# Kernel optimization log

Hardware: AMD Instinct MI355X
Metric: run time of the kernel (lower is better)

## Reference

```python
import jax, jax.numpy as jnp
import numpy as np

N, IN, H, M, C, E = 200000, 256, 256, 64, 64, 3200000

def gelu(x):
    # torch F.gelu default is exact (erf) gelu
    return jax.nn.gelu(x, approximate=False)

def setup_inputs() -> dict:
    key = jax.random.key(0)
    ks = jax.random.split(key, 12)
    s = 0.02  # small init scale for weights
    p = lambda k, shape: jax.random.normal(k, shape, jnp.float32) * s
    inp = {
        "x": jax.random.normal(ks[0], (N, IN), jnp.float32),
        "edge_index": jax.random.randint(ks[1], (2, E), 0, N),
        "ff1_w0": p(ks[2], (IN, H)),   "ff1_b0": jnp.zeros((H,), jnp.float32),
        "wA0":    p(ks[3], (H, H)),    "wB0":    p(ks[4], (H, M)),
        "ff2_w0": p(ks[5], (2 * H, H)),"ff2_b0": jnp.zeros((H,), jnp.float32),
        "ff1_w1": p(ks[6], (H, H)),    "ff1_b1": jnp.zeros((H,), jnp.float32),
        "wA1":    p(ks[7], (H, H)),    "wB1":    p(ks[8], (H, M)),
        "ff2_w1": p(ks[9], (2 * H, H)),"ff2_b1": jnp.zeros((H,), jnp.float32),
        "head_w": p(ks[10], (H, C)),   "head_b": jnp.zeros((C,), jnp.float32),
    }
    return inp

def _ghm_block(X, ff1_w, ff1_b, wA, wB, ff2_w, ff2_b):
    # FF1
    Hf = gelu(X @ ff1_w + ff1_b)                 # (N, h)
    # HyperAggregation: hypernetwork produces token-mixing weights
    W_tar = gelu(Hf @ wA) @ wB                   # (N, m)
    agg = gelu(Hf.T @ W_tar)                     # (h, m) - mixes over nodes
    agg = (agg @ W_tar.T).T                      # (N, h)
    # root connection: concat aggregated with pre-agg features
    agg = gelu(jnp.concatenate([agg, Hf], axis=1))  # (N, 2h)
    return agg @ ff2_w + ff2_b                   # (N, h)

def reference(x, edge_index, ff1_w0, ff1_b0, wA0, wB0, ff2_w0, ff2_b0,
              ff1_w1, ff1_b1, wA1, wB1, ff2_w1, ff2_b1, head_w, head_b):
    # task='graph', batch=None: whole node set is one fully-connected neighborhood
    X = _ghm_block(x, ff1_w0, ff1_b0, wA0, wB0, ff2_w0, ff2_b0)
    X = _ghm_block(X, ff1_w1, ff1_b1, wA1, wB1, ff2_w1, ff2_b1)
    g = jnp.mean(X, axis=0, keepdims=True)       # (1, h)
    return g @ head_w + head_b                   # (1, C)
```

## Files before the change

kernel.cpp:

```cpp
#include <hip/hip_runtime.h>


typedef unsigned short u16;
typedef unsigned int u32;
typedef short bf16x8 __attribute__((ext_vector_type(8)));
typedef float f32x4 __attribute__((ext_vector_type(4)));

__device__ __forceinline__ float gelu_f(float x) {
  float s = x * x;
  float z = x * fmaf(s, -0.10294348f, -2.3022077f);
  float e = __builtin_amdgcn_exp2f(z);
  return x * __builtin_amdgcn_rcpf(1.0f + e);
}
__device__ __forceinline__ u16 f2b(float f) {
  union { float f; unsigned u; } v; v.f = f;
  unsigned u = v.u;
  u += 0x7fffu + ((u >> 16) & 1u);
  return (u16)(u >> 16);
}
__device__ __forceinline__ float b2f(u16 b) {
  union { float f; u32 u; } v; v.u = (u32)b << 16;
  return v.f;
}
__device__ __forceinline__ int swz(int row, int col) {
  return row * 256 + (((col >> 3) ^ (row & 7)) << 3) + (col & 7);
}

__global__ __launch_bounds__(256) void prep_weights(
    const float* __restrict__ s0, const float* __restrict__ s1,
    const float* __restrict__ s2, const float* __restrict__ s3,
    const float* __restrict__ s4, const float* __restrict__ s5,
    const float* __restrict__ s6, const float* __restrict__ s7,
    u16* __restrict__ dst)
{
  int idx = blockIdx.x * 256 + threadIdx.x;
  if (idx >= 557056) return;
  const float* src; int base, R, C;
  if (idx < 278528) {
    if (idx < 131072) {
      if (idx < 65536) { base = 0;      src = s0; R = 256; C = 256; }
      else             { base = 65536;  src = s1; R = 256; C = 256; }
    } else {
      if (idx < 147456){ base = 131072; src = s2; R = 256; C = 64;  }
      else             { base = 147456; src = s3; R = 512; C = 256; }
    }
  } else {
    int j = idx - 278528;
    if (j < 131072) {
      if (j < 65536)   { base = 278528; src = s4; R = 256; C = 256; }
      else             { base = 344064; src = s5; R = 256; C = 256; }
    } else {
      if (j < 147456)  { base = 409600; src = s6; R = 256; C = 64;  }
      else             { base = 425984; src = s7; R = 512; C = 256; }
    }
  }
  int local = idx - base;
  int o = local / R;
  int k = local - o * R;
  dst[idx] = f2b(src[k * C + o]);
}

template<bool AFP32>
__global__ __launch_bounds__(256, 2) void ff1_hyper(
    const void* __restrict__ Av, const u16* __restrict__ W1T,
    const float* __restrict__ bias, const u16* __restrict__ wAT,
    const u16* __restrict__ wBT, u16* __restrict__ Hf,
    u16* __restrict__ Hfg, u16* __restrict__ Wt, int N)
{
  __shared__ u16 Asm[128][264];
  const int tid = threadIdx.x;
  const int wave = tid >> 6, lane = tid & 63;
  int r0 = blockIdx.x * 128;
  if (r0 > N - 128) r0 = N - 128;

  if constexpr (AFP32) {
    const float* A = (const float*)Av;
    #pragma unroll
    for (int j = 0; j < 32; ++j) {
      int idx = j * 256 + tid;
      int row = idx >> 6, c4 = idx & 63;
      float4 v = *(const float4*)(A + (size_t)(r0 + row) * 256 + c4 * 4);
      uint2 p;
      p.x = (u32)f2b(v.x) | ((u32)f2b(v.y) << 16);
      p.y = (u32)f2b(v.z) | ((u32)f2b(v.w) << 16);
      *(uint2*)&Asm[row][c4 * 4] = p;
    }
  } else {
    const u16* A = (const u16*)Av;
    #pragma unroll
    for (int j = 0; j < 16; ++j) {
      int idx = j * 256 + tid;
      int row = idx >> 5, c8 = idx & 31;
      *(uint4*)&Asm[row][c8 * 8] =
          *(const uint4*)(A + (size_t)(r0 + row) * 256 + c8 * 8);
    }
  }
  __syncthreads();

  const int lm = lane & 15, lq = lane >> 4;
  const int n0 = wave * 64;

  f32x4 acc[8][4] = {};
  {
    bf16x8 bb[2][4];
    #pragma unroll
    for (int ct = 0; ct < 4; ++ct)
      bb[0][ct] = *(const bf16x8*)(W1T + (size_t)(n0 + ct * 16 + lm) * 256 + lq * 8);
    #pragma unroll
    for (int s = 0; s < 8; ++s) {
      const int cur = s & 1;
      if (s < 7)
        #pragma unroll
        for (int ct = 0; ct < 4; ++ct)
          bb[cur ^ 1][ct] = *(const bf16x8*)(W1T + (size_t)(n0 + ct * 16 + lm) * 256 + (s + 1) * 32 + lq * 8);
      bf16x8 a[8];
      #pragma unroll
      for (int rt = 0; rt < 8; ++rt)
        a[rt] = *(const bf16x8*)&Asm[rt * 16 + lm][s * 32 + lq * 8];
      #pragma unroll
      for (int rt = 0; rt < 8; ++rt)
        #pragma unroll
        for (int ct = 0; ct < 4; ++ct)
          acc[rt][ct] = __builtin_amdgcn_mfma_f32_16x16x32_bf16(a[rt], bb[cur][ct], acc[rt][ct], 0, 0, 0);
    }
  }
  __syncthreads();

  {
    float bv[4];
    #pragma unroll
    for (int ct = 0; ct < 4; ++ct) bv[ct] = bias[n0 + ct * 16 + lm];
    #pragma unroll
    for (int rt = 0; rt < 8; ++rt)
      #pragma unroll
      for (int ct = 0; ct < 4; ++ct)
        #pragma unroll
        for (int rg = 0; rg < 4; ++rg) {
          float g = gelu_f(acc[rt][ct][rg] + bv[ct]);
          Asm[rt * 16 + lq * 4 + rg][n0 + ct * 16 + lm] = f2b(g);
        }
  }
  __syncthreads();

  #pragma unroll
  for (int j = 0; j < 16; ++j) {
    int idx = j * 256 + tid;
    int row = idx >> 5, c8 = idx & 31;
    uint4 v = *(const uint4*)&Asm[row][c8 * 8];
    *(uint4*)(Hf + (size_t)(r0 + row) * 256 + c8 * 8) = v;
    u32 wsv[4] = {v.x, v.y, v.z, v.w};
    uint4 go;
    u32* gp = (u32*)&go;
    #pragma unroll
    for (int t = 0; t < 4; ++t) {
      float lo = gelu_f(b2f((u16)(wsv[t] & 0xFFFFu)));
      float hi = gelu_f(b2f((u16)(wsv[t] >> 16)));
      gp[t] = (u32)f2b(lo) | ((u32)f2b(hi) << 16);
    }
    *(uint4*)(Hfg + (size_t)(r0 + row) * 256 + c8 * 8) = go;
  }

  #pragma unroll
  for (int rt = 0; rt < 8; ++rt)
    #pragma unroll
    for (int ct = 0; ct < 4; ++ct)
      acc[rt][ct] = (f32x4){0.f, 0.f, 0.f, 0.f};
  {
    bf16x8 bb[2][4];
    #pragma unroll
    for (int ct = 0; ct < 4; ++ct)
      bb[0][ct] = *(const bf16x8*)(wAT + (size_t)(n0 + ct * 16 + lm) * 256 + lq * 8);
    #pragma unroll
    for (int s = 0; s < 8; ++s) {
      const int cur = s & 1;
      if (s < 7)
        #pragma unroll
        for (int ct = 0; ct < 4; ++ct)
          bb[cur ^ 1][ct] = *(const bf16x8*)(wAT + (size_t)(n0 + ct * 16 + lm) * 256 + (s + 1) * 32 + lq * 8);
      bf16x8 a[8];
      #pragma unroll
      for (int rt = 0; rt < 8; ++rt)
        a[rt] = *(const bf16x8*)&Asm[rt * 16 + lm][s * 32 + lq * 8];
      #pragma unroll
      for (int rt = 0; rt < 8; ++rt)
        #pragma unroll
        for (int ct = 0; ct < 4; ++ct)
          acc[rt][ct] = __builtin_amdgcn_mfma_f32_16x16x32_bf16(a[rt], bb[cur][ct], acc[rt][ct], 0, 0, 0);
    }
  }
  __syncthreads();
  #pragma unroll
  for (int rt = 0; rt < 8; ++rt)
    #pragma unroll
    for (int ct = 0; ct < 4; ++ct)
      #pragma unroll
      for (int rg = 0; rg < 4; ++rg)
        Asm[rt * 16 + lq * 4 + rg][n0 + ct * 16 + lm] = f2b(gelu_f(acc[rt][ct][rg]));
  __syncthreads();

  f32x4 acc2[2][4] = {};
  {
    bf16x8 bb[2][4];
    #pragma unroll
    for (int ct = 0; ct < 4; ++ct)
      bb[0][ct] = *(const bf16x8*)(wBT + (size_t)(ct * 16 + lm) * 256 + lq * 8);
    #pragma unroll
    for (int s = 0; s < 8; ++s) {
      const int cur = s & 1;
      if (s < 7)
        #pragma unroll
        for (int ct = 0; ct < 4; ++ct)
          bb[cur ^ 1][ct] = *(const bf16x8*)(wBT + (size_t)(ct * 16 + lm) * 256 + (s + 1) * 32 + lq * 8);
      bf16x8 a[2];
      #pragma unroll
      for (int rt = 0; rt < 2; ++rt)
        a[rt] = *(const bf16x8*)&Asm[wave * 32 + rt * 16 + lm][s * 32 + lq * 8];
      #pragma unroll
      for (int rt = 0; rt < 2; ++rt)
        #pragma unroll
        for (int ct = 0; ct < 4; ++ct)
          acc2[rt][ct] = __builtin_amdgcn_mfma_f32_16x16x32_bf16(a[rt], bb[cur][ct], acc2[rt][ct], 0, 0, 0);
    }
  }
  #pragma unroll
  for (int rt = 0; rt < 2; ++rt)
    #pragma unroll
    for (int ct = 0; ct < 4; ++ct)
      #pragma unroll
      for (int rg = 0; rg < 4; ++rg)
        Asm[wave * 32 + rt * 16 + lq * 4 + rg][ct * 16 + lm] = f2b(acc2[rt][ct][rg]);
  #pragma unroll
  for (int t = 0; t < 4; ++t) {
    int u = t * 64 + lane;
    int rl = u >> 3, c8 = u & 7;
    *(uint4*)(Wt + (size_t)(r0 + wave * 32 + rl) * 64 + c8 * 8) =
        *(const uint4*)&Asm[wave * 32 + rl][c8 * 8];
  }
}

__global__ __launch_bounds__(256, 3) void s_partial_v2(
    const u16* __restrict__ Hf, const u16* __restrict__ Wt,
    float* __restrict__ Spart, int N)
{
  __shared__ u16 HfT[256][72];
  __shared__ u16 WtT[64][72];
  const int tid = threadIdx.x;
  const int wave = tid >> 6, lane = tid & 63;
  const int lm = lane & 15, lq = lane >> 4;
  const int rp = tid & 31;
  const int mb = tid >> 5;
  uint4 hx[4][2], wx[2];
  auto issue = [&](int ch) {
    int i0 = ch << 6;
    #pragma unroll
    for (int q = 0; q < 4; ++q) {
      const u16* px = Hf + (size_t)(i0 + 2 * rp) * 256 + (mb + 8 * q) * 8;
      hx[q][0] = *(const uint4*)px;
      hx[q][1] = *(const uint4*)(px + 256);
    }
    const u16* pw = Wt + (size_t)(i0 + 2 * rp) * 64 + mb * 8;
    wx[0] = *(const uint4*)pw;
    wx[1] = *(const uint4*)(pw + 64);
  };
  f32x4 acc[4][4] = {};
  const int nchunk = N >> 6;
  int ch = blockIdx.x;
  if (ch < nchunk) issue(ch);
  for (; ch < nchunk; ch += gridDim.x) {
    __syncthreads();
    #pragma unroll
    for (int q = 0; q < 4; ++q) {
      int m = mb + 8 * q;
      u32 xs[4] = {hx[q][0].x, hx[q][0].y, hx[q][0].z, hx[q][0].w};
      u32 ys[4] = {hx[q][1].x, hx[q][1].y, hx[q][1].z, hx[q][1].w};
      #pragma unroll
      for (int t = 0; t < 4; ++t) {
        *(u32*)&HfT[m * 8 + 2 * t][2 * rp]     = (xs[t] & 0xFFFFu) | (ys[t] << 16);
        *(u32*)&HfT[m * 8 + 2 * t + 1][2 * rp] = (xs[t] >> 16) | (ys[t] & 0xFFFF0000u);
      }
    }
    {
      u32 xs[4] = {wx[0].x, wx[0].y, wx[0].z, wx[0].w};
      u32 ys[4] = {wx[1].x, wx[1].y, wx[1].z, wx[1].w};
      #pragma unroll
      for (int t = 0; t < 4; ++t) {
        *(u32*)&WtT[mb * 8 + 2 * t][2 * rp]     = (xs[t] & 0xFFFFu) | (ys[t] << 16);
        *(u32*)&WtT[mb * 8 + 2 * t + 1][2 * rp] = (xs[t] >> 16) | (ys[t] & 0xFFFF0000u);
      }
    }
    if (ch + (int)gridDim.x < nchunk) issue(ch + (int)gridDim.x);
    __syncthreads();
    #pragma unroll
    for (int k0 = 0; k0 < 64; k0 += 32) {
      bf16x8 a[4], b[4];
      #pragma unroll
      for (int t = 0; t < 4; ++t)
        a[t] = *(const bf16x8*)&HfT[wave * 64 + t * 16 + lm][k0 + lq * 8];
      #pragma unroll
      for (int m = 0; m < 4; ++m)
        b[m] = *(const bf16x8*)&WtT[m * 16 + lm][k0 + lq * 8];
      #pragma unroll
      for (int t = 0; t < 4; ++t)
        #pragma unroll
        for (int m = 0; m < 4; ++m)
          acc[t][m] = __builtin_amdgcn_mfma_f32_16x16x32_bf16(a[t], b[m], acc[t][m], 0, 0, 0);
    }
  }
  float* out = Spart + (size_t)blockIdx.x * 16384;
  #pragma unroll
  for (int t = 0; t < 4; ++t)
    #pragma unroll
    for (int m = 0; m < 4; ++m)
      #pragma unroll
      for (int rg = 0; rg < 4; ++rg)
        out[(size_t)(wave * 64 + t * 16 + lq * 4 + rg) * 64 + m * 16 + lm] = acc[t][m][rg];
}

__global__ __launch_bounds__(256) void s_reduce(
    const float* __restrict__ Spart, u16* __restrict__ agg, int nparts)
{
  int e = blockIdx.x * 256 + threadIdx.x;
  float s0 = 0.f, s1 = 0.f, s2 = 0.f, s3 = 0.f;
  for (int p = 0; p < nparts; p += 4) {
    s0 += Spart[(size_t)(p + 0) * 16384 + e];
    s1 += Spart[(size_t)(p + 1) * 16384 + e];
    s2 += Spart[(size_t)(p + 2) * 16384 + e];
    s3 += Spart[(size_t)(p + 3) * 16384 + e];
  }
  agg[e] = f2b(gelu_f((s0 + s1) + (s2 + s3)));
}

template<bool COLSUM>
__global__ __launch_bounds__(256, 2) void fused_p_ff2_v6(
    const u16* __restrict__ Wt, const u16* __restrict__ agg,
    const u16* __restrict__ Hfg, const u16* __restrict__ W2T,
    const float* __restrict__ bias, u16* __restrict__ X,
    float* __restrict__ colsum, int N)
{
  __shared__ u16 Hsm[64 * 256];
  __shared__ u16 Pl[64 * 256];
  const int tid = threadIdx.x;
  const int wave = tid >> 6, lane = tid & 63;
  const int lm = lane & 15, lq = lane >> 4;
  const int r0 = blockIdx.x * 64;
  const int n0 = wave * 64;

  #pragma unroll
  for (int t = 0; t < 8; ++t) {
    int unit = (wave * 8 + t) * 64 + lane;
    int row = unit >> 5, ksw = unit & 31;
    int kc = ksw ^ (row & 7);
    const u16* g = Hfg + (size_t)(r0 + row) * 256 + kc * 8;
    __builtin_amdgcn_global_load_lds(
        (const __attribute__((address_space(1))) void*)g,
        (__attribute__((address_space(3))) void*)(Hsm + (size_t)(wave * 8 + t) * 512),
        16, 0, 0);
  }

  auto ldb = [&](int s, bf16x8* b) {
    #pragma unroll
    for (int ct = 0; ct < 4; ++ct)
      b[ct] = *(const bf16x8*)(W2T + (size_t)(n0 + ct * 16 + lm) * 512 + s * 32 + lq * 8);
  };
  auto lda = [&](int s, bf16x8* a) {
    const u16* base = (s < 8) ? Pl : Hsm;
    const int k0 = (s & 7) * 32;
    #pragma unroll
    for (int rt = 0; rt < 4; ++rt) {
      int row = rt * 16 + lm;
      a[rt] = *(const bf16x8*)&base[swz(row, k0 + lq * 8)];
    }
  };

  bf16x8 bb[3][4];
  ldb(0, bb[0]);
  ldb(1, bb[1]);

  {
    f32x4 acc[4][4] = {};
    #pragma unroll
    for (int k0 = 0; k0 < 64; k0 += 32) {
      bf16x8 a[4], b[4];
      #pragma unroll
      for (int ct = 0; ct < 4; ++ct)
        b[ct] = *(const bf16x8*)(agg + (size_t)(n0 + ct * 16 + lm) * 64 + k0 + lq * 8);
      #pragma unroll
      for (int rt = 0; rt < 4; ++rt)
        a[rt] = *(const bf16x8*)(Wt + (size_t)(r0 + rt * 16 + lm) * 64 + k0 + lq * 8);
      #pragma unroll
      for (int rt = 0; rt < 4; ++rt)
        #pragma unroll
        for (int ct = 0; ct < 4; ++ct)
          acc[rt][ct] = __builtin_amdgcn_mfma_f32_16x16x32_bf16(a[rt], b[ct], acc[rt][ct], 0, 0, 0);
    }
    #pragma unroll
    for (int rt = 0; rt < 4; ++rt)
      #pragma unroll
      for (int ct = 0; ct < 4; ++ct)
        #pragma unroll
        for (int rg = 0; rg < 4; ++rg)
          Pl[swz(rt * 16 + lq * 4 + rg, n0 + ct * 16 + lm)] = f2b(gelu_f(acc[rt][ct][rg]));
  }
  __syncthreads();

  f32x4 acc[4][4] = {};
  bf16x8 ab[2][4];
  lda(0, ab[0]);
  #pragma unroll
  for (int s = 0; s < 16; ++s) {
    const int cur = s & 1, nxt = cur ^ 1;
    if (s < 14) ldb(s + 2, bb[(s + 2) % 3]);
    if (s < 15) lda(s + 1, ab[nxt]);
    #pragma unroll
    for (int rt = 0; rt < 4; ++rt)
      #pragma unroll
      for (int ct = 0; ct < 4; ++ct)
        acc[rt][ct] = __builtin_amdgcn_mfma_f32_16x16x32_bf16(ab[cur][rt], bb[s % 3][ct], acc[rt][ct], 0, 0, 0);
  }
  float bv[4];
  #pragma unroll
  for (int ct = 0; ct < 4; ++ct) bv[ct] = bias[n0 + ct * 16 + lm];
  if constexpr (!COLSUM) {
    #pragma unroll
    for (int rt = 0; rt < 4; ++rt)
      #pragma unroll
      for (int ct = 0; ct < 4; ++ct)
        #pragma unroll
        for (int rg = 0; rg < 4; ++rg)
          X[(size_t)(r0 + rt * 16 + lq * 4 + rg) * 256 + n0 + ct * 16 + lm] =
              f2b(acc[rt][ct][rg] + bv[ct]);
  } else {
    #pragma unroll
    for (int ct = 0; ct < 4; ++ct) {
      float cs = 0.0f;
      #pragma unroll
      for (int rt = 0; rt < 4; ++rt)
        #pragma unroll
        for (int rg = 0; rg < 4; ++rg) cs += acc[rt][ct][rg] + bv[ct];
      cs += __shfl_down(cs, 32);
      cs += __shfl_down(cs, 16);
      if (lq == 0) atomicAdd(&colsum[n0 + ct * 16 + lm], cs);
    }
  }
}

__global__ __launch_bounds__(64) void head_kernel(
    const float* __restrict__ colsum, const float* __restrict__ head_w,
    const float* __restrict__ head_b, float* __restrict__ out, float invN)
{
  const int c = threadIdx.x;
  float s = head_b[c];
  for (int h = 0; h < 256; ++h) s = fmaf(colsum[h] * invN, head_w[h * 64 + c], s);
  out[c] = s;
}

extern "C" void kernel_launch(void* const* d_in, const int* in_sizes, int n_in,
                              void* d_out, int out_size, void* d_ws, size_t ws_size,
                              hipStream_t stream)
{
  const float* x        = (const float*)d_in[0];
  const float* ff1_w[2] = {(const float*)d_in[2],  (const float*)d_in[8]};
  const float* ff1_b[2] = {(const float*)d_in[3],  (const float*)d_in[9]};
  const float* wA[2]    = {(const float*)d_in[4],  (const float*)d_in[10]};
  const float* wB[2]    = {(const float*)d_in[5],  (const float*)d_in[11]};
  const float* ff2_w[2] = {(const float*)d_in[6],  (const float*)d_in[12]};
  const float* ff2_b[2] = {(const float*)d_in[7],  (const float*)d_in[13]};
  const float* head_w   = (const float*)d_in[14];
  const float* head_b   = (const float*)d_in[15];
  const int N = in_sizes[0] / 256;

  char* ws = (char*)d_ws;
  u16* WT = (u16*)ws;
  u16* W1T[2] = {WT + 0,      WT + 278528};
  u16* wAT[2] = {WT + 65536,  WT + 344064};
  u16* wBT[2] = {WT + 131072, WT + 409600};
  u16* W2T[2] = {WT + 147456, WT + 425984};
  size_t o = 1114112;
  u16* Hf  = (u16*)(ws + o); o += (size_t)N * 256 * 2;
  u16* Hfg = (u16*)(ws + o); o += (size_t)N * 256 * 2;
  u16* TX  = (u16*)(ws + o); o += (size_t)N * 256 * 2;
  u16* Wt  = (u16*)(ws + o); o += (size_t)N * 64 * 2;
  u16*   agg    = (u16*)(ws + o);   o += 16384 * 2;
  float* colsum = (float*)(ws + o); o += 256 * 4;
  float* Spart = (float*)TX;
  const int NPARTS = 768;
  (void)ws_size; (void)n_in; (void)out_size;

  hipMemsetAsync(colsum, 0, 256 * sizeof(float), stream);
  prep_weights<<<2176, 256, 0, stream>>>(ff1_w[0], wA[0], wB[0], ff2_w[0],
                                         ff1_w[1], wA[1], wB[1], ff2_w[1], WT);
  const int G128 = (N + 127) / 128;
  const int G64  = N / 64;
  ff1_hyper<true><<<G128, 256, 0, stream>>>(x, W1T[0], ff1_b[0], wAT[0], wBT[0], Hf, Hfg, Wt, N);
  s_partial_v2<<<NPARTS, 256, 0, stream>>>(Hf, Wt, Spart, N);
  s_reduce<<<64, 256, 0, stream>>>(Spart, agg, NPARTS);
  fused_p_ff2_v6<false><<<G64, 256, 0, stream>>>(Wt, agg, Hfg, W2T[0], ff2_b[0], TX, nullptr, N);
  ff1_hyper<false><<<G128, 256, 0, stream>>>(TX, W1T[1], ff1_b[1], wAT[1], wBT[1], Hf, Hfg, Wt, N);
  s_partial_v2<<<NPARTS, 256, 0, stream>>>(Hf, Wt, Spart, N);
  s_reduce<<<64, 256, 0, stream>>>(Spart, agg, NPARTS);
  fused_p_ff2_v6<true><<<G64, 256, 0, stream>>>(Wt, agg, Hfg, W2T[1], ff2_b[1], nullptr, colsum, N);
  head_kernel<<<1, 64, 0, stream>>>(colsum, head_w, head_b, (float*)d_out, 1.0f / (float)N);
}
```

Baseline: 1.115 ms.

## Write Hf and Wt pre-transposed and swizzled; DMA them straight into LDS

ff1_hyper now writes Hf and Wt into a chunk-major, transposed, XOR-swizzled layout (64-node chunks) directly from the epilogue registers, instead of row-major Hf. The S partial kernel then uses global_load_lds to copy each chunk straight into double-buffered shared memory, removing the per-chunk register transpose and LDS writes. The partial count drops from 768 to 512. The cost is an extra WtT buffer, scattered 8-byte global stores in ff1_hyper, and a larger LDS footprint per block that may lower occupancy.

Measured after the change: 1.090 ms. 1.02x faster.

```diff
diff --git a/kernel.cpp b/kernel.cpp
--- a/kernel.cpp
+++ b/kernel.cpp
@@ -64,8 +64,8 @@
 __global__ __launch_bounds__(256, 2) void ff1_hyper(
     const void* __restrict__ Av, const u16* __restrict__ W1T,
     const float* __restrict__ bias, const u16* __restrict__ wAT,
-    const u16* __restrict__ wBT, u16* __restrict__ Hf,
-    u16* __restrict__ Hfg, u16* __restrict__ Wt, int N)
+    const u16* __restrict__ wBT, u16* __restrict__ HfT,
+    u16* __restrict__ Hfg, u16* __restrict__ Wt, u16* __restrict__ WtT, int N)
 {
   __shared__ u16 Asm[128][264];
   const int tid = threadIdx.x;
@@ -133,12 +133,24 @@
     #pragma unroll
     for (int rt = 0; rt < 8; ++rt)
       #pragma unroll
-      for (int ct = 0; ct < 4; ++ct)
+      for (int ct = 0; ct < 4; ++ct) {
+        float g[4];
         #pragma unroll
         for (int rg = 0; rg < 4; ++rg) {
-          float g = gelu_f(acc[rt][ct][rg] + bv[ct]);
-          Asm[rt * 16 + lq * 4 + rg][n0 + ct * 16 + lm] = f2b(g);
+          g[rg] = gelu_f(acc[rt][ct][rg] + bv[ct]);
+          Asm[rt * 16 + lq * 4 + rg][n0 + ct * 16 + lm] = f2b(g[rg]);
         }
+        int nb = rt * 16 + lq * 4;
+        int h  = n0 + ct * 16 + lm;
+        int nl = nb & 63;
+        int u  = nl >> 3;
+        int sub= nl & 7;
+        uint2 q;
+        q.x = (u32)f2b(g[0]) | ((u32)f2b(g[1]) << 16);
+        q.y = (u32)f2b(g[2]) | ((u32)f2b(g[3]) << 16);
+        size_t cbase = ((size_t)((r0 + nb) >> 6)) * 16384;
+        *(uint2*)(HfT + cbase + h * 64 + ((u ^ (h & 7)) << 3) + sub) = q;
+      }
   }
   __syncthreads();
 
@@ -147,7 +159,6 @@
     int idx = j * 256 + tid;
     int row = idx >> 5, c8 = idx & 31;
     uint4 v = *(const uint4*)&Asm[row][c8 * 8];
-    *(uint4*)(Hf + (size_t)(r0 + row) * 256 + c8 * 8) = v;
     u32 wsv[4] = {v.x, v.y, v.z, v.w};
     uint4 go;
     u32* gp = (u32*)&go;
@@ -225,10 +236,21 @@
   #pragma unroll
   for (int rt = 0; rt < 2; ++rt)
     #pragma unroll
-    for (int ct = 0; ct < 4; ++ct)
+    for (int ct = 0; ct < 4; ++ct) {
       #pragma unroll
       for (int rg = 0; rg < 4; ++rg)
         Asm[wave * 32 + rt * 16 + lq * 4 + rg][ct * 16 + lm] = f2b(acc2[rt][ct][rg]);
+      int nb = wave * 32 + rt * 16 + lq * 4;
+      int m  = ct * 16 + lm;
+      int nl = nb & 63;
+      int u  = nl >> 3;
+      int sub= nl & 7;
+      uint2 q;
+      q.x = (u32)f2b(acc2[rt][ct][0]) | ((u32)f2b(acc2[rt][ct][1]) << 16);
+      q.y = (u32)f2b(acc2[rt][ct][2]) | ((u32)f2b(acc2[rt][ct][3]) << 16);
+      size_t cbase = ((size_t)((r0 + nb) >> 6)) * 4096;
+      *(uint2*)(WtT + cbase + m * 64 + ((u ^ (m & 7)) << 3) + sub) = q;
+    }
   #pragma unroll
   for (int t = 0; t < 4; ++t) {
     int u = t * 64 + lane;
@@ -238,73 +260,68 @@
   }
 }
 
-__global__ __launch_bounds__(256, 3) void s_partial_v2(
-    const u16* __restrict__ Hf, const u16* __restrict__ Wt,
+__global__ __launch_bounds__(256) void s_partial_v3(
+    const u16* __restrict__ HfT, const u16* __restrict__ WtT,
     float* __restrict__ Spart, int N)
 {
-  __shared__ u16 HfT[256][72];
-  __shared__ u16 WtT[64][72];
+  __shared__ u16 Hbuf[2][256 * 64];
+  __shared__ u16 Wbuf[2][64 * 64];
   const int tid = threadIdx.x;
   const int wave = tid >> 6, lane = tid & 63;
   const int lm = lane & 15, lq = lane >> 4;
-  const int rp = tid & 31;
-  const int mb = tid >> 5;
-  uint4 hx[4][2], wx[2];
-  auto issue = [&](int ch) {
-    int i0 = ch << 6;
-    #pragma unroll
-    for (int q = 0; q < 4; ++q) {
-      const u16* px = Hf + (size_t)(i0 + 2 * rp) * 256 + (mb + 8 * q) * 8;
-      hx[q][0] = *(const uint4*)px;
-      hx[q][1] = *(const uint4*)(px + 256);
-    }
-    const u16* pw = Wt + (size_t)(i0 + 2 * rp) * 64 + mb * 8;
-    wx[0] = *(const uint4*)pw;
-    wx[1] = *(const uint4*)(pw + 64);
+  const int nchunk = N >> 6;
+
+  auto issue = [&](int c, int b) {
+    const u16* gh = HfT + (size_t)c * 16384;
+    #pragma unroll
+    for (int t = 0; t < 8; ++t) {
+      int fi = (t * 4 + wave) * 64;
+      __builtin_amdgcn_global_load_lds(
+          (const __attribute__((address_space(1))) void*)(gh + (size_t)(fi + lane) * 8),
+          (__attribute__((address_space(3))) void*)(&Hbuf[b][fi * 8]),
+          16, 0, 0);
+    }
+    const u16* gw = WtT + (size_t)c * 4096;
+    #pragma unroll
+    for (int t = 0; t < 2; ++t) {
+      int fi = (t * 4 + wave) * 64;
+      __builtin_amdgcn_global_load_lds(
+          (const __attribute__((address_space(1))) void*)(gw + (size_t)(fi + lane) * 8),
+          (__attribute__((address_space(3))) void*)(&Wbuf[b][fi * 8]),
+          16, 0, 0);
+    }
   };
+
   f32x4 acc[4][4] = {};
-  const int nchunk = N >> 6;
+  int buf = 0;
   int ch = blockIdx.x;
-  if (ch < nchunk) issue(ch);
+  if (ch < nchunk) issue(ch, 0);
+  __syncthreads();
   for (; ch < nchunk; ch += gridDim.x) {
-    __syncthreads();
-    #pragma unroll
-    for (int q = 0; q < 4; ++q) {
-      int m = mb + 8 * q;
-      u32 xs[4] = {hx[q][0].x, hx[q][0].y, hx[q][0].z, hx[q][0].w};
-      u32 ys[4] = {hx[q][1].x, hx[q][1].y, hx[q][1].z, hx[q][1].w};
+    int nx = ch + (int)gridDim.x;
+    if (nx < nchunk) issue(nx, buf ^ 1);
+    #pragma unroll
+    for (int k0 = 0; k0 < 64; k0 += 32) {
+      const int ub = (k0 >> 3) + lq;
+      bf16x8 a[4], b[4];
       #pragma unroll
       for (int t = 0; t < 4; ++t) {
-        *(u32*)&HfT[m * 8 + 2 * t][2 * rp]     = (xs[t] & 0xFFFFu) | (ys[t] << 16);
-        *(u32*)&HfT[m * 8 + 2 * t + 1][2 * rp] = (xs[t] >> 16) | (ys[t] & 0xFFFF0000u);
+        int h = wave * 64 + t * 16 + lm;
+        a[t] = *(const bf16x8*)&Hbuf[buf][h * 64 + ((ub ^ (h & 7)) << 3)];
       }
-    }
-    {
-      u32 xs[4] = {wx[0].x, wx[0].y, wx[0].z, wx[0].w};
-      u32 ys[4] = {wx[1].x, wx[1].y, wx[1].z, wx[1].w};
-      #pragma unroll
-      for (int t = 0; t < 4; ++t) {
-        *(u32*)&WtT[mb * 8 + 2 * t][2 * rp]     = (xs[t] & 0xFFFFu) | (ys[t] << 16);
-        *(u32*)&WtT[mb * 8 + 2 * t + 1][2 * rp] = (xs[t] >> 16) | (ys[t] & 0xFFFF0000u);
+      #pragma unroll
+      for (int m = 0; m < 4; ++m) {
+        int mr = m * 16 + lm;
+        b[m] = *(const bf16x8*)&Wbuf[buf][mr * 64 + ((ub ^ (mr & 7)) << 3)];
       }
-    }
-    if (ch + (int)gridDim.x < nchunk) issue(ch + (int)gridDim.x);
-    __syncthreads();
-    #pragma unroll
-    for (int k0 = 0; k0 < 64; k0 += 32) {
-      bf16x8 a[4], b[4];
-      #pragma unroll
-      for (int t = 0; t < 4; ++t)
-        a[t] = *(const bf16x8*)&HfT[wave * 64 + t * 16 + lm][k0 + lq * 8];
-      #pragma unroll
-      for (int m = 0; m < 4; ++m)
-        b[m] = *(const bf16x8*)&WtT[m * 16 + lm][k0 + lq * 8];
       #pragma unroll
       for (int t = 0; t < 4; ++t)
         #pragma unroll
         for (int m = 0; m < 4; ++m)
           acc[t][m] = __builtin_amdgcn_mfma_f32_16x16x32_bf16(a[t], b[m], acc[t][m], 0, 0, 0);
     }
+    __syncthreads();
+    buf ^= 1;
   }
   float* out = Spart + (size_t)blockIdx.x * 16384;
   #pragma unroll
@@ -476,14 +493,15 @@
   u16* wBT[2] = {WT + 131072, WT + 409600};
   u16* W2T[2] = {WT + 147456, WT + 425984};
   size_t o = 1114112;
-  u16* Hf  = (u16*)(ws + o); o += (size_t)N * 256 * 2;
+  u16* HfT = (u16*)(ws + o); o += (size_t)N * 256 * 2;
   u16* Hfg = (u16*)(ws + o); o += (size_t)N * 256 * 2;
   u16* TX  = (u16*)(ws + o); o += (size_t)N * 256 * 2;
   u16* Wt  = (u16*)(ws + o); o += (size_t)N * 64 * 2;
+  u16* WtT = (u16*)(ws + o); o += (size_t)N * 64 * 2;
   u16*   agg    = (u16*)(ws + o);   o += 16384 * 2;
   float* colsum = (float*)(ws + o); o += 256 * 4;
   float* Spart = (float*)TX;
-  const int NPARTS = 768;
+  const int NPARTS = 512;
   (void)ws_size; (void)n_in; (void)out_size;
 
   hipMemsetAsync(colsum, 0, 256 * sizeof(float), stream);
@@ -491,12 +509,12 @@
                                          ff1_w[1], wA[1], wB[1], ff2_w[1], WT);
   const int G128 = (N + 127) / 128;
   const int G64  = N / 64;
-  ff1_hyper<true><<<G128, 256, 0, stream>>>(x, W1T[0], ff1_b[0], wAT[0], wBT[0], Hf, Hfg, Wt, N);
-  s_partial_v2<<<NPARTS, 256, 0, stream>>>(Hf, Wt, Spart, N);
+  ff1_hyper<true><<<G128, 256, 0, stream>>>(x, W1T[0], ff1_b[0], wAT[0], wBT[0], HfT, Hfg, Wt, WtT, N);
+  s_partial_v3<<<NPARTS, 256, 0, stream>>>(HfT, WtT, Spart, N);
   s_reduce<<<64, 256, 0, stream>>>(Spart, agg, NPARTS);
   fused_p_ff2_v6<false><<<G64, 256, 0, stream>>>(Wt, agg, Hfg, W2T[0], ff2_b[0], TX, nullptr, N);
-  ff1_hyper<false><<<G128, 256, 0, stream>>>(TX, W1T[1], ff1_b[1], wAT[1], wBT[1], Hf, Hfg, Wt, N);
-  s_partial_v2<<<NPARTS, 256, 0, stream>>>(Hf, Wt, Spart, N);
+  ff1_hyper<false><<<G128, 256, 0, stream>>>(TX, W1T[1], ff1_b[1], wAT[1], wBT[1], HfT, Hfg, Wt, WtT, N);
+  s_partial_v3<<<NPARTS, 256, 0, stream>>>(HfT, WtT, Spart, N);
   s_reduce<<<64, 256, 0, stream>>>(Spart, agg, NPARTS);
   fused_p_ff2_v6<true><<<G64, 256, 0, stream>>>(Wt, agg, Hfg, W2T[1], ff2_b[1], nullptr, colsum, N);
   head_kernel<<<1, 64, 0, stream>>>(colsum, head_w, head_b, (float*)d_out, 1.0f / (float)N);
```
